# Performance work log

Measured on AMD Instinct MI355X. Metric: run time of the kernel, lower is better.

Reference implementation:

```python
import jax, jax.numpy as jnp
import numpy as np

LN_EPS = 1e-3  # keras LayerNormalization default epsilon


def setup_inputs() -> dict:
    key = jax.random.key(0)
    ks = jax.random.split(key, 6)
    B, H, W, C = 8, 64, 64, 256
    s = 1.0 / np.sqrt(C)
    return {
        "x": jax.random.normal(ks[0], (B, H, W, C), jnp.float32),
        "gamma": jnp.ones((C,), jnp.float32),
        "beta": jnp.zeros((C,), jnp.float32),
        "wq": jax.random.normal(ks[1], (C, C), jnp.float32) * s,
        "bq": jnp.zeros((C,), jnp.float32),
        "wk": jax.random.normal(ks[2], (C, C), jnp.float32) * s,
        "bk": jnp.zeros((C,), jnp.float32),
        "wv": jax.random.normal(ks[3], (C, C), jnp.float32) * s,
        "bv": jnp.zeros((C,), jnp.float32),
        "wo": jax.random.normal(ks[4], (C, C), jnp.float32) * s,
        "bo": jnp.zeros((C,), jnp.float32),
    }


def reference(x, gamma, beta, wq, bq, wk, bk, wv, bv, wo, bo):
    B, H, W, C = x.shape
    # LayerNormalization over channel axis (keras default axis=-1, eps=1e-3)
    mean = jnp.mean(x, axis=-1, keepdims=True)
    var = jnp.mean(jnp.square(x - mean), axis=-1, keepdims=True)
    h = (x - mean) * jax.lax.rsqrt(var + LN_EPS) * gamma + beta

    q = h @ wq + bq
    k = h @ wk + bk
    v = h @ wv + bv

    # flatten spatial dims: single-head attention over N = H*W positions
    N = H * W
    qf = q.reshape(B, N, C)
    kf = k.reshape(B, N, C)
    vf = v.reshape(B, N, C)

    scale = jnp.asarray(C, x.dtype) ** -0.5
    scores = jnp.einsum('bnc,bmc->bnm', qf, kf) * scale  # [B, N, N]
    attn = jax.nn.softmax(scores, axis=-1)
    o = jnp.einsum('bnm,bmc->bnc', attn, vf).reshape(B, H, W, C)

    o = o @ wo + bo
    return x + o
```

## Files before the change

### kernel.cpp

```cpp
#include <hip/hip_runtime.h>
#include <hip/hip_bf16.h>
#include <stdint.h>

typedef __attribute__((ext_vector_type(8))) short bf16x8;
typedef __attribute__((ext_vector_type(4))) short s16x4;
typedef __attribute__((ext_vector_type(4))) float f32x4;

__device__ __forceinline__ unsigned short f2b(float x) {
  __hip_bfloat16 h = __float2bfloat16(x);
  unsigned short u;
  __builtin_memcpy(&u, &h, 2);
  return u;
}

__device__ __forceinline__ float b2f(unsigned short u) {
  unsigned v = (unsigned)u << 16;
  float f;
  __builtin_memcpy(&f, &v, 4);
  return f;
}

__device__ __forceinline__ void glds16(const void* g, void* l) {
  __builtin_amdgcn_global_load_lds((const __attribute__((address_space(1))) void*)g,
                                   (__attribute__((address_space(3))) void*)l,
                                   16, 0, 0);
}

#define LQ_LDS (80 * 1024)

__global__ __launch_bounds__(256, 2) void ln_qkv(
    const float* __restrict__ x, const float* __restrict__ gamma,
    const float* __restrict__ beta, const unsigned short* __restrict__ wT,
    const float* __restrict__ bq, const float* __restrict__ bk,
    const float* __restrict__ bv,
    unsigned short* __restrict__ q, unsigned short* __restrict__ kk,
    unsigned short* __restrict__ vT, float qscale)
{
  extern __shared__ char lds[];
  const int t = threadIdx.x;
  const int lane = t & 63;
  const int w = t >> 6;
  const int wr = w >> 1, wc = w & 1;
  const long long row0 = (long long)blockIdx.y * 128;
  const int col0 = blockIdx.x * 128;

  const int sr = t >> 2;
  const int sc = (t & 3) * 8;

  auto stageB = [&](int st, int c) {
    const unsigned short* gb = wT + (st >> 3) * 65536 +
                               (long long)(col0 + sr) * 256 + (st & 7) * 32 + sc;
    char* d = lds + 65536 + c * 8192 + w * 1024;
    glds16(gb, d);
    glds16(gb + 64 * 256, d + 4096);
  };

  stageB(0, 0);

  {
    const f32x4 g4 = *(const f32x4*)(gamma + lane * 4);
    const f32x4 b4 = *(const f32x4*)(beta + lane * 4);
    for (int rr = 0; rr < 32; rr++) {
      const int rl = w * 32 + rr;
      const f32x4 v = *(const f32x4*)(x + (row0 + rl) * 256 + lane * 4);
      float s = v[0] + v[1] + v[2] + v[3];
      float s2 = v[0] * v[0] + v[1] * v[1] + v[2] * v[2] + v[3] * v[3];
#pragma unroll
      for (int o = 32; o >= 1; o >>= 1) {
        s += __shfl_xor(s, o, 64);
        s2 += __shfl_xor(s2, o, 64);
      }
      const float mean = s * (1.f / 256.f);
      const float var = s2 * (1.f / 256.f) - mean * mean;
      const float rstd = rsqrtf(var + 1e-3f);
      s16x4 hv;
#pragma unroll
      for (int e = 0; e < 4; e++) hv[e] = (short)f2b((v[e] - mean) * rstd * g4[e] + b4[e]);
      *(s16x4*)(lds + ((rl * 512 + lane * 8) ^ ((rl & 7) << 4))) = hv;
    }
  }

  const int l15 = lane & 15;
  const int l4 = lane >> 4;
  int step = 0;
#pragma unroll
  for (int z = 0; z < 3; z++) {
    f32x4 acc[4][4] = {};
#pragma unroll
    for (int k0 = 0; k0 < 8; k0++, step++) {
      const int cur = step & 1;
      __syncthreads();
      if (step < 23) stageB(step + 1, cur ^ 1);
      bf16x8 a[4], b[4];
#pragma unroll
      for (int i = 0; i < 4; i++) {
        const int row = wr * 64 + i * 16 + l15;
        a[i] = *(const bf16x8*)(lds + ((row * 512 + k0 * 64 + l4 * 16) ^ ((l15 & 7) << 4)));
      }
      const char* pb = lds + 65536 + cur * 8192;
#pragma unroll
      for (int j = 0; j < 4; j++)
        b[j] = *(const bf16x8*)(pb + (wc * 64 + j * 16 + l15) * 64 + l4 * 16);
#pragma unroll
      for (int i = 0; i < 4; i++)
#pragma unroll
        for (int j = 0; j < 4; j++)
          acc[i][j] = __builtin_amdgcn_mfma_f32_16x16x32_bf16(a[i], b[j], acc[i][j], 0, 0, 0);
    }
    const float* bias = z == 0 ? bq : z == 1 ? bk : bv;
    const float scale = z == 0 ? qscale : 1.0f;
#pragma unroll
    for (int i = 0; i < 4; i++) {
#pragma unroll
      for (int j = 0; j < 4; j++) {
        const int col = col0 + wc * 64 + j * 16 + l15;
        const float bv_ = bias[col];
#pragma unroll
        for (int r = 0; r < 4; r++) {
          const long long row = row0 + wr * 64 + i * 16 + l4 * 4 + r;
          const float val = (acc[i][j][r] + bv_) * scale;
          if (z == 0) {
            q[row * 256 + col] = f2b(val);
          } else if (z == 1) {
            kk[row * 256 + col] = f2b(val);
          } else {
            const int bb = (int)(row >> 12), rr = (int)(row & 4095);
            const int kl = rr & 31;
            const int rrp = (rr & ~31) |
                            ((((kl >> 2) & 3) << 3) | (((kl >> 4) & 1) << 2) | (kl & 3));
            vT[((long long)bb * 256 + col) * 4096 + rrp] = f2b(val);
          }
        }
      }
    }
  }
}

__global__ __launch_bounds__(256) void gemm_out(
    const unsigned short* __restrict__ o0, const unsigned short* __restrict__ o1,
    const unsigned short* __restrict__ o2, const unsigned short* __restrict__ o3,
    const float2* __restrict__ ml0, const float2* __restrict__ ml1,
    const float2* __restrict__ ml2, const float2* __restrict__ ml3,
    const unsigned short* __restrict__ Bt,
    float* __restrict__ C, const float* __restrict__ bias,
    const float* __restrict__ resid)
{
  __shared__ unsigned short As[128 * 32];
  __shared__ unsigned short Bs[128 * 32];
  const int t = threadIdx.x;
  const int lane = t & 63;
  const int wv_ = t >> 6;
  const int wr = wv_ >> 1, wc = wv_ & 1;
  const long long row0 = (long long)blockIdx.y * 128;
  const int col0 = blockIdx.x * 128;

  const int sr = t >> 2;
  const int sc = (t & 3) * 8;
  const long long ar0 = row0 + sr;
  float fA[2][4];
#pragma unroll
  for (int rr = 0; rr < 2; rr++) {
    const long long row = ar0 + rr * 64;
    const float2 a = ml0[row], c = ml1[row], d = ml2[row], e = ml3[row];
    const float M = fmaxf(fmaxf(a.x, c.x), fmaxf(d.x, e.x));
    const float w0 = exp2f(a.x - M), w1 = exp2f(c.x - M);
    const float w2 = exp2f(d.x - M), w3 = exp2f(e.x - M);
    const float inv = 1.f / (w0 * a.y + w1 * c.y + w2 * d.y + w3 * e.y);
    fA[rr][0] = w0 * inv;
    fA[rr][1] = w1 * inv;
    fA[rr][2] = w2 * inv;
    fA[rr][3] = w3 * inv;
  }
  const unsigned short* g0 = o0 + ar0 * 256 + sc;
  const unsigned short* g1 = o1 + ar0 * 256 + sc;
  const unsigned short* g2 = o2 + ar0 * 256 + sc;
  const unsigned short* g3 = o3 + ar0 * 256 + sc;
  const unsigned short* gb = Bt + (col0 + sr) * 256 + sc;
  char* lB = (char*)Bs + (t >> 6) * 1024;

  const int l15 = lane & 15;
  const int l4 = lane >> 4;
  const unsigned short* pa = As + (wr * 64 + l15) * 32 + l4 * 8;
  const unsigned short* pb = Bs + (wc * 64 + l15) * 32 + l4 * 8;

  f32x4 acc[4][4] = {};

  for (int k0 = 0; k0 < 256; k0 += 32) {
#pragma unroll
    for (int rr = 0; rr < 2; rr++) {
      bf16x8 u0 = *(const bf16x8*)(g0 + rr * 64 * 256);
      bf16x8 u1 = *(const bf16x8*)(g1 + rr * 64 * 256);
      bf16x8 u2 = *(const bf16x8*)(g2 + rr * 64 * 256);
      bf16x8 u3 = *(const bf16x8*)(g3 + rr * 64 * 256);
      bf16x8 m_;
#pragma unroll
      for (int e = 0; e < 8; e++)
        m_[e] = (short)f2b(fA[rr][0] * b2f((unsigned short)u0[e]) +
                           fA[rr][1] * b2f((unsigned short)u1[e]) +
                           fA[rr][2] * b2f((unsigned short)u2[e]) +
                           fA[rr][3] * b2f((unsigned short)u3[e]));
      *(bf16x8*)((char*)As + rr * 4096 + t * 16) = m_;
    }
    glds16(gb, lB);
    glds16(gb + 64 * 256, lB + 4096);
    g0 += 32;
    g1 += 32;
    g2 += 32;
    g3 += 32;
    gb += 32;
    __syncthreads();
    bf16x8 a[4], b[4];
#pragma unroll
    for (int i = 0; i < 4; i++) a[i] = *(const bf16x8*)(pa + i * 512);
#pragma unroll
    for (int j = 0; j < 4; j++) b[j] = *(const bf16x8*)(pb + j * 512);
#pragma unroll
    for (int i = 0; i < 4; i++)
#pragma unroll
      for (int j = 0; j < 4; j++)
        acc[i][j] = __builtin_amdgcn_mfma_f32_16x16x32_bf16(a[i], b[j], acc[i][j], 0, 0, 0);
    __syncthreads();
  }

#pragma unroll
  for (int i = 0; i < 4; i++) {
#pragma unroll
    for (int j = 0; j < 4; j++) {
      const int col = col0 + wc * 64 + j * 16 + l15;
      const float bv_ = bias[col];
#pragma unroll
      for (int r = 0; r < 4; r++) {
        const long long row = row0 + wr * 64 + i * 16 + l4 * 4 + r;
        const long long idx = row * 256 + col;
        C[idx] = resid[idx] + acc[i][j][r] + bv_;
      }
    }
  }
}

__global__ void wtrans(const float* __restrict__ wq, const float* __restrict__ wk,
                       const float* __restrict__ wv, const float* __restrict__ wo,
                       unsigned short* __restrict__ wT)
{
  const float* w = blockIdx.z == 0 ? wq : blockIdx.z == 1 ? wk : blockIdx.z == 2 ? wv : wo;
  unsigned short* o = wT + (long long)blockIdx.z * 65536;
  __shared__ float tile[16][17];
  const int tx = threadIdx.x, ty = threadIdx.y;
  const int bx = blockIdx.x * 16, by = blockIdx.y * 16;
  tile[ty][tx] = w[(by + ty) * 256 + bx + tx];
  __syncthreads();
  o[(bx + ty) * 256 + (by + tx)] = f2b(tile[tx][ty]);
}

#define FL_LDS (32 * 1024)

__global__ __launch_bounds__(256, 2) void flash(
    const unsigned short* __restrict__ q,
    const unsigned short* __restrict__ kk,
    const unsigned short* __restrict__ vT,
    unsigned short* __restrict__ o0, unsigned short* __restrict__ o1,
    unsigned short* __restrict__ o2, unsigned short* __restrict__ o3,
    float2* __restrict__ ml0, float2* __restrict__ ml1,
    float2* __restrict__ ml2, float2* __restrict__ ml3)
{
  extern __shared__ char lds[];
  const int t = threadIdx.x;
  const int w = t >> 6;
  const int lane = t & 63;
  const int l15 = lane & 15, hi = lane >> 4;
  const int b = blockIdx.x & 7;
  const int kh = (blockIdx.x >> 3) & 3;
  const int qb = blockIdx.x >> 5;
  const long long qrow = (long long)b * 4096 + (long long)qb * 128 + w * 32;

  const unsigned short* kbase = kk + (long long)b * 4096 * 256 + (long long)kh * 1024 * 256;
  const unsigned short* vbase = vT + (long long)b * 256 * 4096 + kh * 1024;

  const int gs_k = (t & 31) ^ ((t >> 5) & 7);
  const unsigned short* Kst = kbase + (t >> 5) * 256 + gs_k * 8;
  const int gs_v = (t & 3) ^ ((t >> 2) & 3);
  const unsigned short* Vst = vbase + (long long)(t >> 2) * 4096 + gs_v * 8;

  bf16x8 Qf[2][8];
#pragma unroll
  for (int qg = 0; qg < 2; qg++) {
    const unsigned short* qp = q + (qrow + qg * 16 + l15) * 256 + hi * 8;
#pragma unroll
    for (int ks = 0; ks < 8; ks++) Qf[qg][ks] = *(const bf16x8*)(qp + ks * 32);
  }

  f32x4 O[2][16] = {};
  float mrow[2] = {-1e30f, -1e30f};
  float lrow[2] = {0.f, 0.f};

  auto stage = [&](int it) {
    const unsigned short* ks_ = Kst + (long long)it * 32 * 256;
    const unsigned short* vs_ = Vst + it * 32;
    char* kd = lds + w * 1024;
    char* vd = lds + 16384 + w * 1024;
#pragma unroll
    for (int p = 0; p < 4; p++) {
      glds16(ks_ + p * 8 * 256, kd + p * 4096);
      glds16(vs_ + (long long)p * 64 * 4096, vd + p * 4096);
    }
  };

  stage(0);

  for (int it = 0; it < 32; ++it) {
    asm volatile("s_waitcnt vmcnt(0)" ::: "memory");
    __builtin_amdgcn_sched_barrier(0);
    __builtin_amdgcn_s_barrier();
    const char* Kb = lds;
    const char* Vb = lds + 16384;

    f32x4 S[2][2] = {};
    __builtin_amdgcn_s_setprio(1);
#pragma unroll
    for (int ks = 0; ks < 8; ks++) {
#pragma unroll
      for (int j = 0; j < 2; j++) {
        bf16x8 Kf = *(const bf16x8*)(Kb + (j * 16 + l15) * 512 +
                                     ((ks * 64 + hi * 16) ^ ((l15 & 7) << 4)));
        S[0][j] = __builtin_amdgcn_mfma_f32_16x16x32_bf16(Kf, Qf[0][ks], S[0][j], 0, 0, 0);
        S[1][j] = __builtin_amdgcn_mfma_f32_16x16x32_bf16(Kf, Qf[1][ks], S[1][j], 0, 0, 0);
      }
    }
    __builtin_amdgcn_s_setprio(0);

    bf16x8 Pf8[2];
#pragma unroll
    for (int qg = 0; qg < 2; qg++) {
      const float mxl =
          fmaxf(fmaxf(fmaxf(S[qg][0][0], S[qg][0][1]), fmaxf(S[qg][0][2], S[qg][0][3])),
                fmaxf(fmaxf(S[qg][1][0], S[qg][1][1]), fmaxf(S[qg][1][2], S[qg][1][3])));
      if (!__all(mxl <= mrow[qg] + 8.f)) {
        float mx = fmaxf(mxl, __shfl_xor(mxl, 16, 64));
        mx = fmaxf(mx, __shfl_xor(mx, 32, 64));
        const float mn = fmaxf(mrow[qg], mx);
        const float rs_ = exp2f(mrow[qg] - mn);
        mrow[qg] = mn;
        lrow[qg] *= rs_;
#pragma unroll
        for (int dg = 0; dg < 16; dg++) O[qg][dg] *= rs_;
      }
      float sum = 0.f;
      float e[2][4];
#pragma unroll
      for (int j = 0; j < 2; j++)
#pragma unroll
        for (int r = 0; r < 4; r++) {
          e[j][r] = exp2f(S[qg][j][r] - mrow[qg]);
          sum += e[j][r];
        }
      lrow[qg] += sum;
      bf16x8 p;
#pragma unroll
      for (int j = 0; j < 2; j++)
#pragma unroll
        for (int r = 0; r < 4; r++) p[j * 4 + r] = (short)f2b(e[j][r]);
      Pf8[qg] = p;
    }

    __builtin_amdgcn_s_setprio(1);
#pragma unroll
    for (int dg = 0; dg < 16; dg++) {
      bf16x8 Vf8 = *(const bf16x8*)(Vb + (dg * 16 + l15) * 64 +
                                    ((hi * 16) ^ ((l15 & 3) << 4)));
      O[0][dg] = __builtin_amdgcn_mfma_f32_16x16x32_bf16(Vf8, Pf8[0], O[0][dg], 0, 0, 0);
      O[1][dg] = __builtin_amdgcn_mfma_f32_16x16x32_bf16(Vf8, Pf8[1], O[1][dg], 0, 0, 0);
    }
    __builtin_amdgcn_s_setprio(0);

    __builtin_amdgcn_s_barrier();
    if (it < 31) stage(it + 1);
  }

  unsigned short* const op = kh == 0 ? o0 : kh == 1 ? o1 : kh == 2 ? o2 : o3;
  float2* const mlp = kh == 0 ? ml0 : kh == 1 ? ml1 : kh == 2 ? ml2 : ml3;
  __syncthreads();
  char* const slab = lds + w * 8192;
#pragma unroll
  for (int qg = 0; qg < 2; qg++) {
    float lr = lrow[qg];
    lr += __shfl_xor(lr, 16, 64);
    lr += __shfl_xor(lr, 32, 64);
#pragma unroll
    for (int dg = 0; dg < 16; dg++) {
      s16x4 pk;
#pragma unroll
      for (int r = 0; r < 4; r++) pk[r] = (short)f2b(O[qg][dg][r]);
      *(s16x4*)(slab + l15 * 512 + ((dg * 32 + hi * 8) ^ ((l15 & 7) << 4))) = pk;
    }
    if (hi == 0) mlp[qrow + qg * 16 + l15] = make_float2(mrow[qg], lr);
    const int qq = lane >> 2;
    const int dc = lane & 3;
    const long long orow = (qrow + qg * 16 + qq) * 256 + dc * 64;
#pragma unroll
    for (int st = 0; st < 8; st++) {
      bf16x8 v = *(const bf16x8*)(slab + qq * 512 +
                                  ((dc * 128 + st * 16) ^ ((qq & 7) << 4)));
      *(bf16x8*)(op + orow + st * 8) = v;
    }
    __syncthreads();
  }
}

extern "C" void kernel_launch(void* const* d_in, const int* in_sizes, int n_in,
                              void* d_out, int out_size, void* d_ws, size_t ws_size,
                              hipStream_t stream)
{
  const float* x = (const float*)d_in[0];
  const float* gamma = (const float*)d_in[1];
  const float* beta = (const float*)d_in[2];
  const float* wq = (const float*)d_in[3];
  const float* bq = (const float*)d_in[4];
  const float* wk = (const float*)d_in[5];
  const float* bk = (const float*)d_in[6];
  const float* wv = (const float*)d_in[7];
  const float* bv = (const float*)d_in[8];
  const float* wo = (const float*)d_in[9];
  const float* bo = (const float*)d_in[10];

  const int Cc = 256;
  const long long MR = 32768;

  char* base = (char*)d_ws;
  size_t off = 0;
  auto take = [&](size_t bytes) -> char* {
    char* p = base + off;
    off = (off + bytes + 255) & ~(size_t)255;
    return p;
  };
  unsigned short* q   = (unsigned short*)take((size_t)MR * Cc * 2);
  unsigned short* kk  = (unsigned short*)take((size_t)MR * Cc * 2);
  unsigned short* vT  = (unsigned short*)take((size_t)MR * Cc * 2);
  unsigned short* o0  = (unsigned short*)take((size_t)MR * Cc * 2);
  unsigned short* o1  = (unsigned short*)take((size_t)MR * Cc * 2);
  unsigned short* o2  = (unsigned short*)take((size_t)MR * Cc * 2);
  unsigned short* o3  = (unsigned short*)take((size_t)MR * Cc * 2);
  unsigned short* wT  = (unsigned short*)take(4ull * Cc * Cc * 2);
  float2* ml0 = (float2*)take((size_t)MR * sizeof(float2));
  float2* ml1 = (float2*)take((size_t)MR * sizeof(float2));
  float2* ml2 = (float2*)take((size_t)MR * sizeof(float2));
  float2* ml3 = (float2*)take((size_t)MR * sizeof(float2));

  wtrans<<<dim3(16, 16, 4), dim3(16, 16), 0, stream>>>(wq, wk, wv, wo, wT);

  const float qscale = 0.0625f * 1.44269504f;
  ln_qkv<<<dim3(2, 256), dim3(256), LQ_LDS, stream>>>(x, gamma, beta, wT, bq, bk, bv,
                                                      q, kk, vT, qscale);

  flash<<<dim3(1024), dim3(256), FL_LDS, stream>>>(q, kk, vT, o0, o1, o2, o3,
                                                   ml0, ml1, ml2, ml3);

  gemm_out<<<dim3(2, 256, 1), 256, 0, stream>>>(o0, o1, o2, o3, ml0, ml1, ml2, ml3,
                                                wT + 3 * 65536, (float*)d_out, bo, x);
}
```

Measured before the change: 248.4 us.

## Split keys three ways, halve query tile, double-buffer K loads in flash

The flash kernel now splits the key range into three chunks instead of four and gives each wave 16 query rows instead of 32, launching 1536 blocks. K tiles are double-buffered in a larger LDS allocation, and V is loaded separately with partial vmcnt waits, so K prefetch and V loads overlap compute. The output GEMM merges three partials instead of four. Fewer query rows per wave means less reuse of each K/V tile and more global K/V traffic overall, in exchange for lower register pressure and better load overlap.

```diff
diff --git a/kernel.cpp b/kernel.cpp
--- a/kernel.cpp
+++ b/kernel.cpp
@@ -138,9 +138,9 @@
 
 __global__ __launch_bounds__(256) void gemm_out(
     const unsigned short* __restrict__ o0, const unsigned short* __restrict__ o1,
-    const unsigned short* __restrict__ o2, const unsigned short* __restrict__ o3,
+    const unsigned short* __restrict__ o2,
     const float2* __restrict__ ml0, const float2* __restrict__ ml1,
-    const float2* __restrict__ ml2, const float2* __restrict__ ml3,
+    const float2* __restrict__ ml2,
     const unsigned short* __restrict__ Bt,
     float* __restrict__ C, const float* __restrict__ bias,
     const float* __restrict__ resid)
@@ -157,24 +157,21 @@
   const int sr = t >> 2;
   const int sc = (t & 3) * 8;
   const long long ar0 = row0 + sr;
-  float fA[2][4];
+  float fA[2][3];
 #pragma unroll
   for (int rr = 0; rr < 2; rr++) {
     const long long row = ar0 + rr * 64;
-    const float2 a = ml0[row], c = ml1[row], d = ml2[row], e = ml3[row];
-    const float M = fmaxf(fmaxf(a.x, c.x), fmaxf(d.x, e.x));
-    const float w0 = exp2f(a.x - M), w1 = exp2f(c.x - M);
-    const float w2 = exp2f(d.x - M), w3 = exp2f(e.x - M);
-    const float inv = 1.f / (w0 * a.y + w1 * c.y + w2 * d.y + w3 * e.y);
+    const float2 a = ml0[row], c = ml1[row], d = ml2[row];
+    const float M = fmaxf(fmaxf(a.x, c.x), d.x);
+    const float w0 = exp2f(a.x - M), w1 = exp2f(c.x - M), w2 = exp2f(d.x - M);
+    const float inv = 1.f / (w0 * a.y + w1 * c.y + w2 * d.y);
     fA[rr][0] = w0 * inv;
     fA[rr][1] = w1 * inv;
     fA[rr][2] = w2 * inv;
-    fA[rr][3] = w3 * inv;
   }
   const unsigned short* g0 = o0 + ar0 * 256 + sc;
   const unsigned short* g1 = o1 + ar0 * 256 + sc;
   const unsigned short* g2 = o2 + ar0 * 256 + sc;
-  const unsigned short* g3 = o3 + ar0 * 256 + sc;
   const unsigned short* gb = Bt + (col0 + sr) * 256 + sc;
   char* lB = (char*)Bs + (t >> 6) * 1024;
 
@@ -191,14 +188,12 @@
       bf16x8 u0 = *(const bf16x8*)(g0 + rr * 64 * 256);
       bf16x8 u1 = *(const bf16x8*)(g1 + rr * 64 * 256);
       bf16x8 u2 = *(const bf16x8*)(g2 + rr * 64 * 256);
-      bf16x8 u3 = *(const bf16x8*)(g3 + rr * 64 * 256);
       bf16x8 m_;
 #pragma unroll
       for (int e = 0; e < 8; e++)
         m_[e] = (short)f2b(fA[rr][0] * b2f((unsigned short)u0[e]) +
                            fA[rr][1] * b2f((unsigned short)u1[e]) +
-                           fA[rr][2] * b2f((unsigned short)u2[e]) +
-                           fA[rr][3] * b2f((unsigned short)u3[e]));
+                           fA[rr][2] * b2f((unsigned short)u2[e]));
       *(bf16x8*)((char*)As + rr * 4096 + t * 16) = m_;
     }
     glds16(gb, lB);
@@ -206,7 +201,6 @@
     g0 += 32;
     g1 += 32;
     g2 += 32;
-    g3 += 32;
     gb += 32;
     __syncthreads();
     bf16x8 a[4], b[4];
@@ -252,16 +246,15 @@
   o[(bx + ty) * 256 + (by + tx)] = f2b(tile[tx][ty]);
 }
 
-#define FL_LDS (32 * 1024)
-
-__global__ __launch_bounds__(256, 2) void flash(
+#define FL_LDS (48 * 1024)
+
+__global__ __launch_bounds__(256) void flash(
     const unsigned short* __restrict__ q,
     const unsigned short* __restrict__ kk,
     const unsigned short* __restrict__ vT,
     unsigned short* __restrict__ o0, unsigned short* __restrict__ o1,
-    unsigned short* __restrict__ o2, unsigned short* __restrict__ o3,
-    float2* __restrict__ ml0, float2* __restrict__ ml1,
-    float2* __restrict__ ml2, float2* __restrict__ ml3)
+    unsigned short* __restrict__ o2,
+    float2* __restrict__ ml0, float2* __restrict__ ml1, float2* __restrict__ ml2)
 {
   extern __shared__ char lds[];
   const int t = threadIdx.x;
@@ -269,52 +262,60 @@
   const int lane = t & 63;
   const int l15 = lane & 15, hi = lane >> 4;
   const int b = blockIdx.x & 7;
-  const int kh = (blockIdx.x >> 3) & 3;
-  const int qb = blockIdx.x >> 5;
-  const long long qrow = (long long)b * 4096 + (long long)qb * 128 + w * 32;
-
-  const unsigned short* kbase = kk + (long long)b * 4096 * 256 + (long long)kh * 1024 * 256;
-  const unsigned short* vbase = vT + (long long)b * 256 * 4096 + kh * 1024;
+  const int rem = blockIdx.x >> 3;
+  const int kh = rem % 3;
+  const int qb = rem / 3;
+  const int nit = (kh == 2) ? 42 : 43;
+  const int kbeg = kh * 1376;
+  const long long qrow = (long long)b * 4096 + (long long)qb * 64 + w * 16;
+
+  const unsigned short* kbase = kk + (long long)b * 4096 * 256 + (long long)kbeg * 256;
+  const unsigned short* vbase = vT + (long long)b * 256 * 4096 + kbeg;
 
   const int gs_k = (t & 31) ^ ((t >> 5) & 7);
   const unsigned short* Kst = kbase + (t >> 5) * 256 + gs_k * 8;
   const int gs_v = (t & 3) ^ ((t >> 2) & 3);
   const unsigned short* Vst = vbase + (long long)(t >> 2) * 4096 + gs_v * 8;
 
-  bf16x8 Qf[2][8];
-#pragma unroll
-  for (int qg = 0; qg < 2; qg++) {
-    const unsigned short* qp = q + (qrow + qg * 16 + l15) * 256 + hi * 8;
-#pragma unroll
-    for (int ks = 0; ks < 8; ks++) Qf[qg][ks] = *(const bf16x8*)(qp + ks * 32);
-  }
-
-  f32x4 O[2][16] = {};
-  float mrow[2] = {-1e30f, -1e30f};
-  float lrow[2] = {0.f, 0.f};
-
-  auto stage = [&](int it) {
+  bf16x8 Qf[8];
+  {
+    const unsigned short* qp = q + (qrow + l15) * 256 + hi * 8;
+#pragma unroll
+    for (int ks = 0; ks < 8; ks++) Qf[ks] = *(const bf16x8*)(qp + ks * 32);
+  }
+
+  f32x4 O[16] = {};
+  float mrow = -1e30f;
+  float lrow = 0.f;
+
+  auto stageK = [&](int it, int c) {
     const unsigned short* ks_ = Kst + (long long)it * 32 * 256;
+    char* kd = lds + c * 16384 + w * 1024;
+#pragma unroll
+    for (int p = 0; p < 4; p++) glds16(ks_ + p * 8 * 256, kd + p * 4096);
+  };
+  auto stageV = [&](int it) {
     const unsigned short* vs_ = Vst + it * 32;
-    char* kd = lds + w * 1024;
-    char* vd = lds + 16384 + w * 1024;
-#pragma unroll
-    for (int p = 0; p < 4; p++) {
-      glds16(ks_ + p * 8 * 256, kd + p * 4096);
-      glds16(vs_ + (long long)p * 64 * 4096, vd + p * 4096);
-    }
+    char* vd = lds + 32768 + w * 1024;
+#pragma unroll
+    for (int p = 0; p < 4; p++) glds16(vs_ + (long long)p * 64 * 4096, vd + p * 4096);
   };
 
-  stage(0);
-
-  for (int it = 0; it < 32; ++it) {
-    asm volatile("s_waitcnt vmcnt(0)" ::: "memory");
+  stageK(0, 0);
+
+  for (int it = 0; it < nit; ++it) {
+    const int cur = it & 1;
+    __builtin_amdgcn_s_barrier();
+    stageV(it);
+    const int nxt = (it + 1 < nit) ? it + 1 : it;
+    stageK(nxt, cur ^ 1);
+    asm volatile("s_waitcnt vmcnt(8)" ::: "memory");
     __builtin_amdgcn_sched_barrier(0);
     __builtin_amdgcn_s_barrier();
-    const char* Kb = lds;
-    const char* Vb = lds + 16384;
-
-    f32x4 S[2][2] = {};
+    const char* Kb = lds + cur * 16384;
+    const char* Vb = lds + 32768;
+
+    f32x4 S[2] = {};
     __builtin_amdgcn_s_setprio(1);
 #pragma unroll
     for (int ks = 0; ks < 8; ks++) {
@@ -322,27 +323,24 @@
       for (int j = 0; j < 2; j++) {
         bf16x8 Kf = *(const bf16x8*)(Kb + (j * 16 + l15) * 512 +
                                      ((ks * 64 + hi * 16) ^ ((l15 & 7) << 4)));
-        S[0][j] = __builtin_amdgcn_mfma_f32_16x16x32_bf16(Kf, Qf[0][ks], S[0][j], 0, 0, 0);
-        S[1][j] = __builtin_amdgcn_mfma_f32_16x16x32_bf16(Kf, Qf[1][ks], S[1][j], 0, 0, 0);
+        S[j] = __builtin_amdgcn_mfma_f32_16x16x32_bf16(Kf, Qf[ks], S[j], 0, 0, 0);
       }
     }
     __builtin_amdgcn_s_setprio(0);
 
-    bf16x8 Pf8[2];
-#pragma unroll
-    for (int qg = 0; qg < 2; qg++) {
-      const float mxl =
-          fmaxf(fmaxf(fmaxf(S[qg][0][0], S[qg][0][1]), fmaxf(S[qg][0][2], S[qg][0][3])),
-                fmaxf(fmaxf(S[qg][1][0], S[qg][1][1]), fmaxf(S[qg][1][2], S[qg][1][3])));
-      if (!__all(mxl <= mrow[qg] + 8.f)) {
+    bf16x8 Pf8;
+    {
+      const float mxl = fmaxf(fmaxf(fmaxf(S[0][0], S[0][1]), fmaxf(S[0][2], S[0][3])),
+                              fmaxf(fmaxf(S[1][0], S[1][1]), fmaxf(S[1][2], S[1][3])));
+      if (!__all(mxl <= mrow + 8.f)) {
         float mx = fmaxf(mxl, __shfl_xor(mxl, 16, 64));
         mx = fmaxf(mx, __shfl_xor(mx, 32, 64));
-        const float mn = fmaxf(mrow[qg], mx);
-        const float rs_ = exp2f(mrow[qg] - mn);
-        mrow[qg] = mn;
-        lrow[qg] *= rs_;
-#pragma unroll
-        for (int dg = 0; dg < 16; dg++) O[qg][dg] *= rs_;
+        const float mn = fmaxf(mrow, mx);
+        const float rs_ = exp2f(mrow - mn);
+        mrow = mn;
+        lrow *= rs_;
+#pragma unroll
+        for (int dg = 0; dg < 16; dg++) O[dg] *= rs_;
       }
       float sum = 0.f;
       float e[2][4];
@@ -350,59 +348,57 @@
       for (int j = 0; j < 2; j++)
 #pragma unroll
         for (int r = 0; r < 4; r++) {
-          e[j][r] = exp2f(S[qg][j][r] - mrow[qg]);
+          e[j][r] = exp2f(S[j][r] - mrow);
           sum += e[j][r];
         }
-      lrow[qg] += sum;
+      lrow += sum;
       bf16x8 p;
 #pragma unroll
       for (int j = 0; j < 2; j++)
 #pragma unroll
         for (int r = 0; r < 4; r++) p[j * 4 + r] = (short)f2b(e[j][r]);
-      Pf8[qg] = p;
-    }
+      Pf8 = p;
+    }
+
+    asm volatile("s_waitcnt vmcnt(4)" ::: "memory");
+    __builtin_amdgcn_sched_barrier(0);
+    __builtin_amdgcn_s_barrier();
 
     __builtin_amdgcn_s_setprio(1);
 #pragma unroll
     for (int dg = 0; dg < 16; dg++) {
       bf16x8 Vf8 = *(const bf16x8*)(Vb + (dg * 16 + l15) * 64 +
                                     ((hi * 16) ^ ((l15 & 3) << 4)));
-      O[0][dg] = __builtin_amdgcn_mfma_f32_16x16x32_bf16(Vf8, Pf8[0], O[0][dg], 0, 0, 0);
-      O[1][dg] = __builtin_amdgcn_mfma_f32_16x16x32_bf16(Vf8, Pf8[1], O[1][dg], 0, 0, 0);
+      O[dg] = __builtin_amdgcn_mfma_f32_16x16x32_bf16(Vf8, Pf8, O[dg], 0, 0, 0);
     }
     __builtin_amdgcn_s_setprio(0);
-
-    __builtin_amdgcn_s_barrier();
-    if (it < 31) stage(it + 1);
-  }
-
-  unsigned short* const op = kh == 0 ? o0 : kh == 1 ? o1 : kh == 2 ? o2 : o3;
-  float2* const mlp = kh == 0 ? ml0 : kh == 1 ? ml1 : kh == 2 ? ml2 : ml3;
+  }
+
+  unsigned short* const op = kh == 0 ? o0 : kh == 1 ? o1 : o2;
+  float2* const mlp = kh == 0 ? ml0 : kh == 1 ? ml1 : ml2;
   __syncthreads();
   char* const slab = lds + w * 8192;
-#pragma unroll
-  for (int qg = 0; qg < 2; qg++) {
-    float lr = lrow[qg];
+  {
+    float lr = lrow;
     lr += __shfl_xor(lr, 16, 64);
     lr += __shfl_xor(lr, 32, 64);
 #pragma unroll
     for (int dg = 0; dg < 16; dg++) {
       s16x4 pk;
 #pragma unroll
-      for (int r = 0; r < 4; r++) pk[r] = (short)f2b(O[qg][dg][r]);
+      for (int r = 0; r < 4; r++) pk[r] = (short)f2b(O[dg][r]);
       *(s16x4*)(slab + l15 * 512 + ((dg * 32 + hi * 8) ^ ((l15 & 7) << 4))) = pk;
     }
-    if (hi == 0) mlp[qrow + qg * 16 + l15] = make_float2(mrow[qg], lr);
+    if (hi == 0) mlp[qrow + l15] = make_float2(mrow, lr);
     const int qq = lane >> 2;
     const int dc = lane & 3;
-    const long long orow = (qrow + qg * 16 + qq) * 256 + dc * 64;
+    const long long orow = (qrow + qq) * 256 + dc * 64;
 #pragma unroll
     for (int st = 0; st < 8; st++) {
       bf16x8 v = *(const bf16x8*)(slab + qq * 512 +
                                   ((dc * 128 + st * 16) ^ ((qq & 7) << 4)));
       *(bf16x8*)(op + orow + st * 8) = v;
     }
-    __syncthreads();
   }
 }
 
@@ -438,12 +434,10 @@
   unsigned short* o0  = (unsigned short*)take((size_t)MR * Cc * 2);
   unsigned short* o1  = (unsigned short*)take((size_t)MR * Cc * 2);
   unsigned short* o2  = (unsigned short*)take((size_t)MR * Cc * 2);
-  unsigned short* o3  = (unsigned short*)take((size_t)MR * Cc * 2);
   unsigned short* wT  = (unsigned short*)take(4ull * Cc * Cc * 2);
   float2* ml0 = (float2*)take((size_t)MR * sizeof(float2));
   float2* ml1 = (float2*)take((size_t)MR * sizeof(float2));
   float2* ml2 = (float2*)take((size_t)MR * sizeof(float2));
-  float2* ml3 = (float2*)take((size_t)MR * sizeof(float2));
 
   wtrans<<<dim3(16, 16, 4), dim3(16, 16), 0, stream>>>(wq, wk, wv, wo, wT);
 
@@ -451,9 +445,8 @@
   ln_qkv<<<dim3(2, 256), dim3(256), LQ_LDS, stream>>>(x, gamma, beta, wT, bq, bk, bv,
                                                       q, kk, vT, qscale);
 
-  flash<<<dim3(1024), dim3(256), FL_LDS, stream>>>(q, kk, vT, o0, o1, o2, o3,
-                                                   ml0, ml1, ml2, ml3);
-
-  gemm_out<<<dim3(2, 256, 1), 256, 0, stream>>>(o0, o1, o2, o3, ml0, ml1, ml2, ml3,
+  flash<<<dim3(1536), dim3(256), FL_LDS, stream>>>(q, kk, vT, o0, o1, o2, ml0, ml1, ml2);
+
+  gemm_out<<<dim3(2, 256, 1), 256, 0, stream>>>(o0, o1, o2, ml0, ml1, ml2,
                                                 wT + 3 * 65536, (float*)d_out, bo, x);
 }
```

Measured after the change: 270.9 us. 1.09x slower.
